# Optimization experiments

Measured on AMD Instinct MI355X. Metric: run time of the kernel, lower is better.

## Reference

```python
import jax, jax.numpy as jnp
import numpy as np

B, C, NNEG, D = 4096, 5, 20, 128
NUM_EMB = 400000  # vocab * num_poly


def setup_inputs() -> dict:
    key = jax.random.key(0)
    k1, k2, k3, k4, k5 = jax.random.split(key, 5)
    iword = jax.random.randint(k1, (B,), 0, NUM_EMB, dtype=jnp.int64)
    owords = jax.random.randint(k2, (B, C), 0, NUM_EMB, dtype=jnp.int64)
    nwords = jax.random.randint(k3, (B, C * NNEG), 0, NUM_EMB, dtype=jnp.int64)
    emb1 = jax.random.normal(k4, (NUM_EMB, D), dtype=jnp.float32) * 0.1
    emb2 = jax.random.normal(k5, (NUM_EMB, D), dtype=jnp.float32) * 0.1
    return {"iword": iword, "owords": owords, "nwords": nwords,
            "emb1": emb1, "emb2": emb2}


def reference(iword, owords, nwords, emb1, emb2):
    v1 = emb1[iword]          # [B, D] center vectors
    v2 = emb2[owords]         # [B, C, D] context vectors
    vn = emb2[nwords]         # [B, C*NNEG, D] negative vectors
    # positive: mean over context of log sigmoid(v2 . v1)
    o_scores = jnp.einsum('bcd,bd->bc', v2, v1)
    oloss = jax.nn.log_sigmoid(o_scores).mean(axis=1)              # [B]
    # negatives: vectors are negated -> log sigmoid(-score), sum over negs, mean over context
    n_scores = jnp.einsum('bkd,bd->bk', vn, v1)                    # [B, C*NNEG]
    nloss = jax.nn.log_sigmoid(-n_scores).reshape(-1, C, NNEG).sum(axis=2).mean(axis=1)  # [B]
    return -(oloss + nloss).mean()
```

## Files before the change

### kernel.cpp

```cpp
#include <hip/hip_runtime.h>
#include <math.h>

#define B 4096
#define C 5
#define NNEG 20
#define D 128
#define NROWS (C + C * NNEG)

__device__ __forceinline__ float log_sigmoid(float x) {
    return fminf(x, 0.0f) - log1pf(__expf(-fabsf(x)));
}

__global__ __launch_bounds__(256) void sgns_partial(
    const int* __restrict__ iword,
    const int* __restrict__ owords,
    const int* __restrict__ nwords,
    const float* __restrict__ emb1,
    const float* __restrict__ emb2,
    float* __restrict__ partial)
{
    const int b    = blockIdx.x;
    const int tid  = threadIdx.x;
    const int lane = tid & 63;
    const int wave = tid >> 6;

    const long center = (long)iword[b] * D;
    const float2 v1 = *(const float2*)(emb1 + center + 2 * lane);

    float acc = 0.0f;
    for (int r = wave; r < NROWS; r += 4) {
        const bool pos = (r < C);
        long idx;
        if (pos) idx = owords[b * C + r];
        else     idx = nwords[b * (C * NNEG) + (r - C)];

        const float2 row = *(const float2*)(emb2 + idx * D + 2 * lane);
        float s = v1.x * row.x + v1.y * row.y;

        #pragma unroll
        for (int off = 32; off > 0; off >>= 1)
            s += __shfl_xor(s, off, 64);

        acc += log_sigmoid(pos ? s : -s);
    }

    __shared__ float wsum[4];
    if (lane == 0) wsum[wave] = acc;
    __syncthreads();
    if (tid == 0) partial[b] = wsum[0] + wsum[1] + wsum[2] + wsum[3];
}

__global__ __launch_bounds__(256) void sgns_reduce(
    const float* __restrict__ partial,
    float* __restrict__ out)
{
    const int tid = threadIdx.x;
    float acc = 0.0f;
    for (int i = tid; i < B; i += 256) acc += partial[i];

    #pragma unroll
    for (int off = 32; off > 0; off >>= 1)
        acc += __shfl_xor(acc, off, 64);

    __shared__ float ws[4];
    if ((tid & 63) == 0) ws[tid >> 6] = acc;
    __syncthreads();
    if (tid == 0) out[0] = -(ws[0] + ws[1] + ws[2] + ws[3]) / (float)(B * C);
}

extern "C" void kernel_launch(void* const* d_in, const int* in_sizes, int n_in,
                              void* d_out, int out_size, void* d_ws, size_t ws_size,
                              hipStream_t stream) {
    const int*   iword  = (const int*)d_in[0];
    const int*   owords = (const int*)d_in[1];
    const int*   nwords = (const int*)d_in[2];
    const float* emb1   = (const float*)d_in[3];
    const float* emb2   = (const float*)d_in[4];
    float* out     = (float*)d_out;
    float* partial = (float*)d_ws;

    sgns_partial<<<B, 256, 0, stream>>>(iword, owords, nwords, emb1, emb2, partial);
    sgns_reduce<<<1, 256, 0, stream>>>(partial, out);
}
```

Measured before the change: 411.2 us.

## Map eight lanes per gathered row with float4 loads and unrolled passes

Each wave now processes eight embedding rows at once, with eight lanes per row. Each lane reads four float4 chunks of the row. The row loop is unrolled into four fixed passes, so many independent gathers can be in flight per wave instead of one row per iteration. The per-row reduction drops to three shuffles. Each lane's sum is then replicated across its 8-lane group, so the block total is scaled by 1/8 to compensate. The cost is more registers per thread and some idle lanes in the last pass.

```diff
diff --git a/kernel.cpp b/kernel.cpp
--- a/kernel.cpp
+++ b/kernel.cpp
@@ -23,31 +23,52 @@
     const int tid  = threadIdx.x;
     const int lane = tid & 63;
     const int wave = tid >> 6;
+    const int grp  = lane >> 3;
+    const int j    = lane & 7;
 
     const long center = (long)iword[b] * D;
-    const float2 v1 = *(const float2*)(emb1 + center + 2 * lane);
+    const float4* v1p = (const float4*)(emb1 + center);
+    float4 v1f[4];
+    #pragma unroll
+    for (int k = 0; k < 4; ++k) v1f[k] = v1p[j + 8 * k];
 
     float acc = 0.0f;
-    for (int r = wave; r < NROWS; r += 4) {
-        const bool pos = (r < C);
-        long idx;
-        if (pos) idx = owords[b * C + r];
-        else     idx = nwords[b * (C * NNEG) + (r - C)];
 
-        const float2 row = *(const float2*)(emb2 + idx * D + 2 * lane);
-        float s = v1.x * row.x + v1.y * row.y;
+    #pragma unroll
+    for (int pass = 0; pass < 4; ++pass) {
+        const int r = pass * 32 + wave * 8 + grp;
+        if (r < NROWS) {
+            const bool pos = (r < C);
+            long idx;
+            if (pos) idx = owords[b * C + r];
+            else     idx = nwords[b * (C * NNEG) + (r - C)];
 
-        #pragma unroll
-        for (int off = 32; off > 0; off >>= 1)
-            s += __shfl_xor(s, off, 64);
+            const float4* rp = (const float4*)(emb2 + idx * D);
+            float s = 0.0f;
+            #pragma unroll
+            for (int k = 0; k < 4; ++k) {
+                const float4 rw = rp[j + 8 * k];
+                s += v1f[k].x * rw.x + v1f[k].y * rw.y
+                   + v1f[k].z * rw.z + v1f[k].w * rw.w;
+            }
 
-        acc += log_sigmoid(pos ? s : -s);
+            s += __shfl_xor(s, 1, 64);
+            s += __shfl_xor(s, 2, 64);
+            s += __shfl_xor(s, 4, 64);
+
+            acc += log_sigmoid(pos ? s : -s);
+        }
     }
+
+    #pragma unroll
+    for (int off = 32; off > 0; off >>= 1)
+        acc += __shfl_xor(acc, off, 64);
 
     __shared__ float wsum[4];
     if (lane == 0) wsum[wave] = acc;
     __syncthreads();
-    if (tid == 0) partial[b] = wsum[0] + wsum[1] + wsum[2] + wsum[3];
+    if (tid == 0)
+        partial[b] = (wsum[0] + wsum[1] + wsum[2] + wsum[3]) * 0.125f;
 }
 
 __global__ __launch_bounds__(256) void sgns_reduce(
```

New measurement: 357.4 us. 13.1% less time.
